# Performance work log

Hardware: AMD Instinct MI355X
Metric: run time of the kernel (lower is better)

## Reference

```python
import jax, jax.numpy as jnp
import numpy as np

LATENT = 64
COND = 768
HEADS = 8
R = 8           # LoRA rank
SCALING = 1.0   # lora_alpha / r
SCALE = (LATENT / HEADS) ** -0.5


def _lora_linear(x, W, b, A, B):
    # loralib-style: y = x W^T + b + scaling * (x A^T) B^T
    return x @ W.T + b + SCALING * ((x @ A.T) @ B.T)


def setup_inputs() -> dict:
    key = jax.random.key(0)
    ks = jax.random.split(key, 20)
    B, C, H, W_ = 16, LATENT, 64, 64
    L = 77
    z = jax.random.normal(ks[0], (B, C, H, W_), dtype=jnp.float32)
    cond = jax.random.normal(ks[1], (B, L, COND), dtype=jnp.float32)

    def lin(k, out_d, in_d):
        k1, k2, k3 = jax.random.split(k, 3)
        W = jax.random.normal(k1, (out_d, in_d), dtype=jnp.float32) * 0.02
        b = jnp.zeros((out_d,), dtype=jnp.float32)
        A = jax.random.normal(k2, (R, in_d), dtype=jnp.float32) * 0.02
        Bm = jax.random.normal(k3, (out_d, R), dtype=jnp.float32) * 0.02
        return W, b, A, Bm

    Wq, bq, Aq, Bq = lin(ks[2], LATENT, LATENT)
    Wk, bk, Ak, Bk = lin(ks[3], LATENT, COND)
    Wv, bv, Av, Bv = lin(ks[4], LATENT, COND)
    Wo, bo, Ao, Bo = lin(ks[5], LATENT, LATENT)
    return dict(z=z, cond=cond,
                Wq=Wq, bq=bq, Aq=Aq, Bq=Bq,
                Wk=Wk, bk=bk, Ak=Ak, Bk=Bk,
                Wv=Wv, bv=bv, Av=Av, Bv=Bv,
                Wo=Wo, bo=bo, Ao=Ao, Bo=Bo)


def reference(z, cond, Wq, bq, Aq, Bq, Wk, bk, Ak, Bk, Wv, bv, Av, Bv, Wo, bo, Ao, Bo):
    B, C, H, W_ = z.shape
    hw = H * W_
    dh = C // HEADS
    z_flat = z.transpose(0, 2, 3, 1).reshape(B, hw, C)  # [B, hw, C]

    q = _lora_linear(z_flat, Wq, bq, Aq, Bq)   # [B, hw, C]
    k = _lora_linear(cond, Wk, bk, Ak, Bk)     # [B, L, C]
    v = _lora_linear(cond, Wv, bv, Av, Bv)     # [B, L, C]

    q = q.reshape(B, hw, HEADS, dh).transpose(0, 2, 1, 3)  # [B, h, hw, dh]
    k = k.reshape(B, -1, HEADS, dh).transpose(0, 2, 1, 3)  # [B, h, L, dh]
    v = v.reshape(B, -1, HEADS, dh).transpose(0, 2, 1, 3)

    dots = jnp.einsum('bhqd,bhkd->bhqk', q, k) * SCALE  # [B, h, hw, L]
    attn = jax.nn.softmax(dots, axis=-1)
    out = jnp.einsum('bhqk,bhkd->bhqd', attn, v)        # [B, h, hw, dh]
    out = out.transpose(0, 2, 1, 3).reshape(B, hw, C)
    out = _lora_linear(out, Wo, bo, Ao, Bo)
    return out.reshape(B, H, W_, C).transpose(0, 3, 1, 2)  # [B, C, H, W]
```

## Files before the change

### kernel.cpp

```cpp
#include <hip/hip_runtime.h>


#define HW   4096
#define CHN  64
#define LSEQ 77
#define CD   768
#define NB   16

#define OFF_WQ 0
#define OFF_WK 4096
#define OFF_WV 53248
#define OFF_WO 102400
#define OFF_K  106496
#define OFF_V  185344
#define OFF_PA 264192

#define QF 0.51011784563163f

__global__ __launch_bounds__(256) void prep_weights(
    const float* __restrict__ Wq, const float* __restrict__ Aq, const float* __restrict__ Bq,
    const float* __restrict__ Wk, const float* __restrict__ Ak, const float* __restrict__ Bk,
    const float* __restrict__ Wv, const float* __restrict__ Av, const float* __restrict__ Bv,
    const float* __restrict__ Wo, const float* __restrict__ Ao, const float* __restrict__ Bo,
    float* __restrict__ ws) {
  int idx = blockIdx.x * 256 + threadIdx.x;
  const float *W, *A, *Bm;
  float* out;
  int in_d, local;
  float scale = 1.0f;
  if (idx < 4096)        { W = Wq; A = Aq; Bm = Bq; out = ws + OFF_WQ; in_d = 64;  local = idx; scale = QF; }
  else if (idx < 53248)  { W = Wk; A = Ak; Bm = Bk; out = ws + OFF_WK; in_d = 768; local = idx - 4096; }
  else if (idx < 102400) { W = Wv; A = Av; Bm = Bv; out = ws + OFF_WV; in_d = 768; local = idx - 53248; }
  else                   { W = Wo; A = Ao; Bm = Bo; out = ws + OFF_WO; in_d = 64;  local = idx - 102400; }
  int co = local & 63;
  int c  = local >> 6;
  float val = W[co * in_d + c];
  #pragma unroll
  for (int r = 0; r < 8; r++) val += Bm[co * 8 + r] * A[r * in_d + c];
  out[local] = val * scale;
}

__global__ __launch_bounds__(128, 2) void kvproj(
    const float* __restrict__ cond,
    const float* __restrict__ wkT,
    const float* __restrict__ wvT,
    float* __restrict__ part) {
  int chunk = blockIdx.x;
  int kv    = blockIdx.y;
  int b     = blockIdx.z;
  int l     = threadIdx.x;
  if (l >= LSEQ) return;
  const float* wT = kv ? wvT : wkT;
  int c0 = chunk * 64;
  const float* xr = cond + (b * LSEQ + l) * CD + c0;
  float zr[64];
  #pragma unroll
  for (int i = 0; i < 16; i++) {
    float4 t4 = ((const float4*)xr)[i];
    zr[4*i] = t4.x; zr[4*i+1] = t4.y; zr[4*i+2] = t4.z; zr[4*i+3] = t4.w;
  }
  float acc[64];
  #pragma unroll
  for (int co = 0; co < 64; co++) acc[co] = 0.f;
  #pragma unroll 4
  for (int c = 0; c < 64; c++) {
    float zv = zr[c];
    #pragma unroll
    for (int co = 0; co < 64; co++) acc[co] = fmaf(zv, wT[(c0 + c) * 64 + co], acc[co]);
  }
  float* pout = part + (((kv * 12 + chunk) * NB + b) * LSEQ + l) * 64;
  #pragma unroll
  for (int i = 0; i < 16; i++) {
    ((float4*)pout)[i] = make_float4(acc[4*i], acc[4*i+1], acc[4*i+2], acc[4*i+3]);
  }
}

__global__ __launch_bounds__(256) void kvreduce(
    const float* __restrict__ part,
    const float* __restrict__ bk, const float* __restrict__ bv,
    float* __restrict__ kbuf, float* __restrict__ vbuf) {
  int idx = blockIdx.x * 256 + threadIdx.x;
  int kv = idx / (NB * LSEQ * 64);
  int r  = idx - kv * (NB * LSEQ * 64);
  int co = idx & 63;
  float val = kv ? bv[co] : bk[co];
  #pragma unroll
  for (int ch = 0; ch < 12; ch++)
    val += part[(kv * 12 + ch) * (NB * LSEQ * 64) + r];
  (kv ? vbuf : kbuf)[r] = val;
}

__global__ __launch_bounds__(256, 2) void megattn(
    const float* __restrict__ z,
    const float* __restrict__ wqT,
    const float* __restrict__ bq,
    const float* __restrict__ kbuf,
    const float* __restrict__ vbuf,
    const float* __restrict__ woT,
    const float* __restrict__ bo,
    float* __restrict__ out) {
  __shared__ float smem[LSEQ * 64 * 2];
  int b  = blockIdx.y;
  int p0 = blockIdx.x * 128;
  int t  = threadIdx.x;
  int h  = t >> 5;
  int pl = t & 31;

  float* ks = smem;
  float* vs = smem + LSEQ * 64;
  {
    const float4* ksrc = (const float4*)(kbuf + b * LSEQ * 64);
    const float4* vsrc = (const float4*)(vbuf + b * LSEQ * 64);
    float4* kd = (float4*)ks;
    float4* vd = (float4*)vs;
    for (int i = t; i < LSEQ * 16; i += 256) { kd[i] = ksrc[i]; vd[i] = vsrc[i]; }
  }

  float qr[4][8];
  {
    const float4 b0 = *(const float4*)(bq + 8 * h);
    const float4 b1 = *(const float4*)(bq + 8 * h + 4);
    #pragma unroll
    for (int i = 0; i < 4; i++) {
      qr[i][0] = b0.x * QF; qr[i][1] = b0.y * QF; qr[i][2] = b0.z * QF; qr[i][3] = b0.w * QF;
      qr[i][4] = b1.x * QF; qr[i][5] = b1.y * QF; qr[i][6] = b1.z * QF; qr[i][7] = b1.w * QF;
    }
  }
  const float* zb = z + b * (CHN * HW) + p0 + pl;
  #pragma unroll 4
  for (int c = 0; c < 64; c++) {
    float4 w0 = *(const float4*)(wqT + c * 64 + 8 * h);
    float4 w1 = *(const float4*)(wqT + c * 64 + 8 * h + 4);
    float zv[4];
    #pragma unroll
    for (int i = 0; i < 4; i++) zv[i] = zb[c * HW + 32 * i];
    #pragma unroll
    for (int i = 0; i < 4; i++) {
      qr[i][0] = fmaf(zv[i], w0.x, qr[i][0]);
      qr[i][1] = fmaf(zv[i], w0.y, qr[i][1]);
      qr[i][2] = fmaf(zv[i], w0.z, qr[i][2]);
      qr[i][3] = fmaf(zv[i], w0.w, qr[i][3]);
      qr[i][4] = fmaf(zv[i], w1.x, qr[i][4]);
      qr[i][5] = fmaf(zv[i], w1.y, qr[i][5]);
      qr[i][6] = fmaf(zv[i], w1.z, qr[i][6]);
      qr[i][7] = fmaf(zv[i], w1.w, qr[i][7]);
    }
  }
  __syncthreads();

  float acc[4][8];
  float li[4];
  #pragma unroll
  for (int i = 0; i < 4; i++) {
    li[i] = 0.f;
    #pragma unroll
    for (int d = 0; d < 8; d++) acc[i][d] = 0.f;
  }
  #pragma unroll 2
  for (int j = 0; j < LSEQ; j++) {
    float4 k0 = *(const float4*)(ks + j * 64 + 8 * h);
    float4 k1 = *(const float4*)(ks + j * 64 + 8 * h + 4);
    float4 v0 = *(const float4*)(vs + j * 64 + 8 * h);
    float4 v1 = *(const float4*)(vs + j * 64 + 8 * h + 4);
    #pragma unroll
    for (int i = 0; i < 4; i++) {
      float s = qr[i][0] * k0.x;
      s = fmaf(qr[i][1], k0.y, s);
      s = fmaf(qr[i][2], k0.z, s);
      s = fmaf(qr[i][3], k0.w, s);
      s = fmaf(qr[i][4], k1.x, s);
      s = fmaf(qr[i][5], k1.y, s);
      s = fmaf(qr[i][6], k1.z, s);
      s = fmaf(qr[i][7], k1.w, s);
      float e = __builtin_amdgcn_exp2f(s);
      li[i] += e;
      acc[i][0] = fmaf(e, v0.x, acc[i][0]);
      acc[i][1] = fmaf(e, v0.y, acc[i][1]);
      acc[i][2] = fmaf(e, v0.z, acc[i][2]);
      acc[i][3] = fmaf(e, v0.w, acc[i][3]);
      acc[i][4] = fmaf(e, v1.x, acc[i][4]);
      acc[i][5] = fmaf(e, v1.y, acc[i][5]);
      acc[i][6] = fmaf(e, v1.z, acc[i][6]);
      acc[i][7] = fmaf(e, v1.w, acc[i][7]);
    }
  }
  __syncthreads();

  float* ao = smem;
  #pragma unroll
  for (int i = 0; i < 4; i++) {
    float inv = 1.0f / li[i];
    int p = pl + 32 * i;
    #pragma unroll
    for (int d = 0; d < 8; d++) ao[p * 65 + 8 * h + d] = acc[i][d] * inv;
  }
  __syncthreads();

  int q2 = t & 127;
  int chalf = __builtin_amdgcn_readfirstlane((t >> 7) & 1);
  float acc2[32];
  #pragma unroll
  for (int j2 = 0; j2 < 32; j2++) acc2[j2] = bo[chalf * 32 + j2];
  const float* aor = ao + q2 * 65;
  #pragma unroll 4
  for (int c = 0; c < 64; c++) {
    float xv = aor[c];
    const float* wr = woT + c * 64 + chalf * 32;
    #pragma unroll
    for (int j2 = 0; j2 < 32; j2++) acc2[j2] = fmaf(xv, wr[j2], acc2[j2]);
  }
  float* ob = out + b * (CHN * HW) + p0 + q2;
  #pragma unroll
  for (int j2 = 0; j2 < 32; j2++) ob[(chalf * 32 + j2) * HW] = acc2[j2];
}

extern "C" void kernel_launch(void* const* d_in, const int* in_sizes, int n_in,
                              void* d_out, int out_size, void* d_ws, size_t ws_size,
                              hipStream_t stream) {
  const float* z    = (const float*)d_in[0];
  const float* cond = (const float*)d_in[1];
  const float* Wq = (const float*)d_in[2];  const float* bq = (const float*)d_in[3];
  const float* Aq = (const float*)d_in[4];  const float* Bq = (const float*)d_in[5];
  const float* Wk = (const float*)d_in[6];  const float* bk = (const float*)d_in[7];
  const float* Ak = (const float*)d_in[8];  const float* Bk = (const float*)d_in[9];
  const float* Wv = (const float*)d_in[10]; const float* bv = (const float*)d_in[11];
  const float* Av = (const float*)d_in[12]; const float* Bv = (const float*)d_in[13];
  const float* Wo = (const float*)d_in[14]; const float* bo = (const float*)d_in[15];
  const float* Ao = (const float*)d_in[16]; const float* Bo = (const float*)d_in[17];
  float* ws  = (float*)d_ws;
  float* out = (float*)d_out;

  prep_weights<<<416, 256, 0, stream>>>(Wq, Aq, Bq, Wk, Ak, Bk, Wv, Av, Bv, Wo, Ao, Bo, ws);
  kvproj<<<dim3(12, 2, 16), 128, 0, stream>>>(cond, ws + OFF_WK, ws + OFF_WV, ws + OFF_PA);
  kvreduce<<<616, 256, 0, stream>>>(ws + OFF_PA, bk, bv, ws + OFF_K, ws + OFF_V);
  megattn<<<dim3(32, 16), 256, 0, stream>>>(z, ws + OFF_WQ, bq, ws + OFF_K, ws + OFF_V,
                                            ws + OFF_WO, bo, out);
}
```

Measured before the change: 179.3 us.

## Replace split-K KV projection and reduce with single direct projection kernel

Drops the two-pass K/V projection, where per-chunk partial sums were written to workspace and then summed by a separate reduce kernel, in favour of one kernel. In the new kernel each wavefront computes one full output row, one thread per output channel, and loops over all 768 inputs with the bias folded in. This removes one launch and the round trip of partial sums through global memory. In exchange each thread runs a long serial FMA chain, and the cond row loads are the same for every lane of a wavefront, so they may be served mostly from cache.

```diff
diff --git a/kernel.cpp b/kernel.cpp
--- a/kernel.cpp
+++ b/kernel.cpp
@@ -13,7 +13,6 @@
 #define OFF_WO 102400
 #define OFF_K  106496
 #define OFF_V  185344
-#define OFF_PA 264192
 
 #define QF 0.51011784563163f
 
@@ -40,54 +39,30 @@
   out[local] = val * scale;
 }
 
-__global__ __launch_bounds__(128, 2) void kvproj(
+__global__ __launch_bounds__(512, 4) void kvproj2(
     const float* __restrict__ cond,
     const float* __restrict__ wkT,
     const float* __restrict__ wvT,
-    float* __restrict__ part) {
-  int chunk = blockIdx.x;
-  int kv    = blockIdx.y;
-  int b     = blockIdx.z;
-  int l     = threadIdx.x;
-  if (l >= LSEQ) return;
+    const float* __restrict__ bk, const float* __restrict__ bv,
+    float* __restrict__ kbuf,
+    float* __restrict__ vbuf) {
+  int kv = blockIdx.y;
+  int t  = threadIdx.x;
+  int w  = __builtin_amdgcn_readfirstlane(t >> 6);
+  int co = t & 63;
+  int row = blockIdx.x * 8 + w;
   const float* wT = kv ? wvT : wkT;
-  int c0 = chunk * 64;
-  const float* xr = cond + (b * LSEQ + l) * CD + c0;
-  float zr[64];
-  #pragma unroll
-  for (int i = 0; i < 16; i++) {
-    float4 t4 = ((const float4*)xr)[i];
-    zr[4*i] = t4.x; zr[4*i+1] = t4.y; zr[4*i+2] = t4.z; zr[4*i+3] = t4.w;
-  }
-  float acc[64];
-  #pragma unroll
-  for (int co = 0; co < 64; co++) acc[co] = 0.f;
-  #pragma unroll 4
-  for (int c = 0; c < 64; c++) {
-    float zv = zr[c];
-    #pragma unroll
-    for (int co = 0; co < 64; co++) acc[co] = fmaf(zv, wT[(c0 + c) * 64 + co], acc[co]);
-  }
-  float* pout = part + (((kv * 12 + chunk) * NB + b) * LSEQ + l) * 64;
-  #pragma unroll
-  for (int i = 0; i < 16; i++) {
-    ((float4*)pout)[i] = make_float4(acc[4*i], acc[4*i+1], acc[4*i+2], acc[4*i+3]);
-  }
-}
-
-__global__ __launch_bounds__(256) void kvreduce(
-    const float* __restrict__ part,
-    const float* __restrict__ bk, const float* __restrict__ bv,
-    float* __restrict__ kbuf, float* __restrict__ vbuf) {
-  int idx = blockIdx.x * 256 + threadIdx.x;
-  int kv = idx / (NB * LSEQ * 64);
-  int r  = idx - kv * (NB * LSEQ * 64);
-  int co = idx & 63;
-  float val = kv ? bv[co] : bk[co];
-  #pragma unroll
-  for (int ch = 0; ch < 12; ch++)
-    val += part[(kv * 12 + ch) * (NB * LSEQ * 64) + r];
-  (kv ? vbuf : kbuf)[r] = val;
+  const float* xr = cond + row * CD;
+  float acc = (kv ? bv : bk)[co];
+  #pragma unroll 8
+  for (int c4 = 0; c4 < CD / 4; c4++) {
+    float4 xv = *(const float4*)(xr + 4 * c4);
+    acc = fmaf(xv.x, wT[(4 * c4 + 0) * 64 + co], acc);
+    acc = fmaf(xv.y, wT[(4 * c4 + 1) * 64 + co], acc);
+    acc = fmaf(xv.z, wT[(4 * c4 + 2) * 64 + co], acc);
+    acc = fmaf(xv.w, wT[(4 * c4 + 3) * 64 + co], acc);
+  }
+  (kv ? vbuf : kbuf)[row * 64 + co] = acc;
 }
 
 __global__ __launch_bounds__(256, 2) void megattn(
@@ -231,8 +206,8 @@
   float* out = (float*)d_out;
 
   prep_weights<<<416, 256, 0, stream>>>(Wq, Aq, Bq, Wk, Ak, Bk, Wv, Av, Bv, Wo, Ao, Bo, ws);
-  kvproj<<<dim3(12, 2, 16), 128, 0, stream>>>(cond, ws + OFF_WK, ws + OFF_WV, ws + OFF_PA);
-  kvreduce<<<616, 256, 0, stream>>>(ws + OFF_PA, bk, bv, ws + OFF_K, ws + OFF_V);
+  kvproj2<<<dim3(154, 2), 512, 0, stream>>>(cond, ws + OFF_WK, ws + OFF_WV, bk, bv,
+                                            ws + OFF_K, ws + OFF_V);
   megattn<<<dim3(32, 16), 256, 0, stream>>>(z, ws + OFF_WQ, bq, ws + OFF_K, ws + OFF_V,
                                             ws + OFF_WO, bo, out);
 }
```

After: 169.0 us. 5.8% less time.
